# Performance work log

Measured on AMD Instinct MI355X. Metric: run time of the kernel, lower is better.

Reference implementation:

```python
import jax, jax.numpy as jnp
import numpy as np

B, INPUT, HIDDEN, K = 16384, 3072, 1024, 128
D = HIDDEN // K          # latents per sample
NUM_EMB = K              # NearestEmbed(k, k): codebook (emb_dim=K, num_emb=K)


def setup_inputs() -> dict:
    key = jax.random.key(0)
    ks = jax.random.split(key, 6)
    def lin(k, o, i):
        s = 1.0 / np.sqrt(i)
        return jax.random.uniform(k, (o, i), jnp.float32, -s, s)
    return {
        'x':  jax.random.uniform(ks[0], (B, INPUT), jnp.float32),  # image-like in [0,1)
        'W1': lin(ks[1], 400, INPUT),   'b1': jnp.zeros((400,), jnp.float32),
        'W2': lin(ks[2], HIDDEN, 400),  'b2': jnp.zeros((HIDDEN,), jnp.float32),
        'W3': lin(ks[3], 400, HIDDEN),  'b3': jnp.zeros((400,), jnp.float32),
        'W4': lin(ks[4], INPUT, 400),   'b4': jnp.zeros((INPUT,), jnp.float32),
        'W_emb': jax.random.uniform(ks[5], (K, NUM_EMB), jnp.float32),  # torch.rand init
    }


def quantize(x, W):
    # x: (B, K, D) with the embedding dim on axis 1; W: (K, nE)
    # squared distance expansion == argmin of torch.norm over dim 1
    d = (x * x).sum(1)[:, :, None] \
        - 2.0 * jnp.einsum('bkd,kn->bdn', x, W) \
        + (W * W).sum(0)[None, None, :]          # (B, D, nE)
    idx = jnp.argmin(d, axis=-1)                  # (B, D)
    zq = jnp.transpose(W.T[idx], (0, 2, 1))       # gather -> (B, D, K) -> (B, K, D)
    return zq, idx


def reference(x, W1, b1, W2, b2, W3, b3, W4, b4, W_emb):
    # encode
    h1 = jax.nn.relu(x @ W1.T + b1)
    z_e = (h1 @ W2.T + b2).reshape(B, K, D)
    # VQ lookups (weight_sg / input-detach only matter for backward)
    z_q, _ = quantize(z_e, W_emb)
    emb_o, _ = quantize(z_e, W_emb)
    # decode (flatten latents back to hidden, as the math requires)
    h3 = jax.nn.relu(z_q.reshape(B, HIDDEN) @ W3.T + b3)
    recon = jax.nn.sigmoid(h3 @ W4.T + b4)
    return recon, z_e, emb_o
```

## Files before the change

### kernel.cpp

```cpp
#include <hip/hip_runtime.h>
#include <math.h>


typedef short bf16x8 __attribute__((ext_vector_type(8)));
typedef short short8 __attribute__((ext_vector_type(8)));
typedef float f32x4  __attribute__((ext_vector_type(4)));

#define GAP_T   2e-4
#define FIX_CAP 4096

__device__ __forceinline__ unsigned short f32_to_bf16_rn(float v) {
    union { float f; unsigned u; } c; c.f = v;
    unsigned r = c.u + 0x7FFFu + ((c.u >> 16) & 1u);
    return (unsigned short)(r >> 16);
}
__device__ __forceinline__ float bf16_bits_to_f32(unsigned short b) {
    union { unsigned u; float f; } c; c.u = ((unsigned)b) << 16;
    return c.f;
}
__device__ __forceinline__ void glds16(const short* g, short* l) {
    __builtin_amdgcn_global_load_lds(
        (const __attribute__((address_space(1))) unsigned int*)g,
        (__attribute__((address_space(3))) unsigned int*)l, 16, 0, 0);
}
__device__ __forceinline__ size_t zq_plane_off(int id, int ii) {
    const int mb = id >> 7, r = id & 127;
    const int kt = ii >> 5, kc = ii & 31;
    return ((size_t)(mb * 32 + kt) * 4096)
         + r * 32 + (((kc >> 3) ^ (r & 3)) << 3) + (kc & 7);
}

__global__ __launch_bounds__(256) void prep_all(
    const float* __restrict__ x,
    const float* __restrict__ W1, const float* __restrict__ W2,
    const float* __restrict__ W3, const float* __restrict__ W4,
    const float* __restrict__ Wemb,
    short* __restrict__ xh,  short* __restrict__ xl,
    short* __restrict__ w1h, short* __restrict__ w1l,
    short* __restrict__ w2h, short* __restrict__ w2l,
    short* __restrict__ w3h, short* __restrict__ w4h,
    short* __restrict__ wembpl, double* __restrict__ wn,
    int* __restrict__ flag_cnt)
{
    const int tid = threadIdx.x;
    int bid = blockIdx.x;

    if (bid < 12288) {
        const int kt = bid % 96;
        const int mb = bid / 96;
        const size_t tb = (size_t)bid * 4096;
        for (int ci = tid; ci < 512; ci += 256) {
            const int row = ci >> 2;
            const int sl  = ci & 3;
            const int k0  = ((sl ^ (row & 3)) << 3);
            const float* src = &x[(size_t)(mb * 128 + row) * 3072 + kt * 32 + k0];
            const float4 f0 = *reinterpret_cast<const float4*>(src);
            const float4 f1 = *reinterpret_cast<const float4*>(src + 4);
            const float ff[8] = {f0.x, f0.y, f0.z, f0.w, f1.x, f1.y, f1.z, f1.w};
            short8 h, l;
            #pragma unroll
            for (int e = 0; e < 8; ++e) {
                const unsigned short hb = f32_to_bf16_rn(ff[e]);
                h[e] = (short)hb;
                l[e] = (short)f32_to_bf16_rn(ff[e] - bf16_bits_to_f32(hb));
            }
            *reinterpret_cast<short8*>(&xh[tb + ci * 8]) = h;
            *reinterpret_cast<short8*>(&xl[tb + ci * 8]) = l;
        }
        return;
    }
    bid -= 12288;

    if (bid < 928) {
        const float* Wsrc; int N, K, KT, local; short *hi, *lo;
        if (bid < 384)      { Wsrc = W1; N = 400;  K = 3072; KT = 96; local = bid;       hi = w1h; lo = w1l; }
        else if (bid < 488) { Wsrc = W2; N = 1024; K = 400;  KT = 13; local = bid - 384; hi = w2h; lo = w2l; }
        else if (bid < 616) { Wsrc = W3; N = 400;  K = 1024; KT = 32; local = bid - 488; hi = w3h; lo = nullptr; }
        else                { Wsrc = W4; N = 3072; K = 400;  KT = 13; local = bid - 616; hi = w4h; lo = nullptr; }

        const int kt = local % KT;
        const int nb = local / KT;
        const size_t tb = (size_t)local * 4096;
        for (int ci = tid; ci < 512; ci += 256) {
            const int row = ci >> 2;
            const int sl  = ci & 3;
            const int k0  = ((sl ^ (row & 3)) << 3);
            const int n   = nb * 128 + row;
            const int kk  = kt * 32 + k0;
            float f[8];
            #pragma unroll
            for (int e = 0; e < 8; ++e)
                f[e] = (n < N && kk + e < K) ? Wsrc[(size_t)n * K + kk + e] : 0.f;
            short8 h, l;
            #pragma unroll
            for (int e = 0; e < 8; ++e) {
                const unsigned short hb = f32_to_bf16_rn(f[e]);
                h[e] = (short)hb;
                l[e] = (short)f32_to_bf16_rn(f[e] - bf16_bits_to_f32(hb));
            }
            *reinterpret_cast<short8*>(&hi[tb + ci * 8]) = h;
            if (lo) *reinterpret_cast<short8*>(&lo[tb + ci * 8]) = l;
        }
        return;
    }

    if (tid == 0) *flag_cnt = 0;
    if (tid < 128) {
        double s = 0.0;
        for (int k = 0; k < 128; ++k) {
            const double w = (double)Wemb[k * 128 + tid];
            s = fma(w, w, s);
        }
        wn[tid] = s;
    }
    for (int t = tid; t < 16384; t += 256) {
        const int k = t >> 7, n = t & 127;
        const float w = Wemb[t];
        const unsigned short hi = f32_to_bf16_rn(w);
        const unsigned short lo = f32_to_bf16_rn(w - bf16_bits_to_f32(hi));
        const int off = n * 128 + (((k >> 3) ^ (n & 7)) << 3) + (k & 7);
        wembpl[off]         = (short)hi;
        wembpl[16384 + off] = (short)lo;
    }
}

template<int NSPLIT, int ACT, int OUTMODE>
__global__ __launch_bounds__(256) void gemm_pl(
    const short* __restrict__ Ahi, const short* __restrict__ Alo,
    const short* __restrict__ Bhi, const short* __restrict__ Blo,
    const float* __restrict__ bias,
    float* __restrict__ Cf32, short* __restrict__ Cphi, short* __restrict__ Cplo,
    int N, int KT, int KTout)
{
    __shared__ short lds[2 * NSPLIT * 2 * 4096];

    const int tid  = threadIdx.x;
    const int lane = tid & 63;
    const int w_id = tid >> 6;
    const int wr   = (w_id >> 1) * 64;
    const int wc   = (w_id & 1)  * 64;
    const int m0   = blockIdx.y * 128;
    const int n0   = blockIdx.x * 128;
    const int l15  = lane & 15;
    const int lg   = lane >> 4;
    constexpr int BUF = NSPLIT * 2 * 4096;

    f32x4 acc[4][4];
    #pragma unroll
    for (int i = 0; i < 4; ++i)
        #pragma unroll
        for (int j = 0; j < 4; ++j) acc[i][j] = (f32x4){0.f, 0.f, 0.f, 0.f};

    auto stage = [&](int buf, int kt) {
        short* L = &lds[buf * BUF];
        const size_t at = ((size_t)blockIdx.y * KT + kt) * 4096;
        const size_t bt = ((size_t)blockIdx.x * KT + kt) * 4096;
        #pragma unroll
        for (int q = 0; q < 2; ++q) {
            const int o = (w_id * 2 + q) * 512 + lane * 8;
            glds16(Ahi + at + o, &L[o]);
            if (NSPLIT > 1) glds16(Alo + at + o, &L[4096 + o]);
            glds16(Bhi + bt + o, &L[NSPLIT * 4096 + o]);
            if (NSPLIT > 1) glds16(Blo + bt + o, &L[(NSPLIT + 1) * 4096 + o]);
        }
    };

    stage(0, 0);
    __syncthreads();

    int cur = 0;
    for (int kt = 0; kt < KT; ++kt) {
        if (kt + 1 < KT) stage(cur ^ 1, kt + 1);

        const short* L = &lds[cur * BUF];
        bf16x8 bfr[4][NSPLIT];
        #pragma unroll
        for (int fc = 0; fc < 4; ++fc) {
            const int rn  = wc + fc * 16 + l15;
            const int idx = rn * 32 + ((lg ^ (rn & 3)) << 3);
            #pragma unroll
            for (int s = 0; s < NSPLIT; ++s)
                bfr[fc][s] = *reinterpret_cast<const bf16x8*>(&L[(NSPLIT + s) * 4096 + idx]);
        }
        #pragma unroll
        for (int fr = 0; fr < 4; ++fr) {
            const int rm  = wr + fr * 16 + l15;
            const int idx = rm * 32 + ((lg ^ (rm & 3)) << 3);
            const bf16x8 a0 = *reinterpret_cast<const bf16x8*>(&L[idx]);
            bf16x8 a1;
            if (NSPLIT > 1)
                a1 = *reinterpret_cast<const bf16x8*>(&L[4096 + idx]);
            #pragma unroll
            for (int fc = 0; fc < 4; ++fc) {
                acc[fr][fc] = __builtin_amdgcn_mfma_f32_16x16x32_bf16(
                    a0, bfr[fc][0], acc[fr][fc], 0, 0, 0);
                if (NSPLIT > 1) {
                    acc[fr][fc] = __builtin_amdgcn_mfma_f32_16x16x32_bf16(
                        a0, bfr[fc][1], acc[fr][fc], 0, 0, 0);
                    acc[fr][fc] = __builtin_amdgcn_mfma_f32_16x16x32_bf16(
                        a1, bfr[fc][0], acc[fr][fc], 0, 0, 0);
                }
            }
        }
        __syncthreads();
        cur ^= 1;
    }

    float bv[4];
    #pragma unroll
    for (int fc = 0; fc < 4; ++fc) {
        const int col = n0 + wc + fc * 16 + l15;
        bv[fc] = (col < N) ? bias[col] : 0.f;
    }
    #pragma unroll
    for (int fr = 0; fr < 4; ++fr) {
        #pragma unroll
        for (int fc = 0; fc < 4; ++fc) {
            const int col = n0 + wc + fc * 16 + l15;
            #pragma unroll
            for (int j = 0; j < 4; ++j) {
                const int rowg = m0 + wr + fr * 16 + lg * 4 + j;
                float v = acc[fr][fc][j] + bv[fc];
                if (ACT == 1) v = fmaxf(v, 0.f);
                else if (ACT == 2) v = 1.f / (1.f + expf(-v));
                if (OUTMODE == 0) {
                    if (col < N) Cf32[(size_t)rowg * N + col] = v;
                } else {
                    const int kto = col >> 5;
                    if (kto < KTout) {
                        const int r = rowg & 127, k = col & 31;
                        const size_t off = ((size_t)blockIdx.y * KTout + kto) * 4096
                                         + r * 32 + (((k >> 3) ^ (r & 3)) << 3) + (k & 7);
                        const unsigned short hb = f32_to_bf16_rn(v);
                        Cphi[off] = (short)hb;
                        if (OUTMODE == 2)
                            Cplo[off] = (short)f32_to_bf16_rn(v - bf16_bits_to_f32(hb));
                    }
                }
            }
        }
    }
}

__global__ __launch_bounds__(512) void vq_mfma(
    const float* __restrict__ z_e, const short* __restrict__ planes,
    const double* __restrict__ wn_g, float* __restrict__ zq,
    short* __restrict__ zqh,
    int* __restrict__ flag_cnt, int* __restrict__ flag_ids)
{
    __shared__ short  Wsh[32768];
    __shared__ float  zsh[16 * 1024];
    __shared__ double wn_sh[128];
    __shared__ double cmb_v1[128][2];
    __shared__ double cmb_v2[128][2];
    __shared__ int    cmb_i[128][2];
    __shared__ int    idx_sh[128];
    __shared__ int    sflag[16];

    const int tid = threadIdx.x;
    const int b0  = blockIdx.x * 16;

    for (int c = tid; c < 4096; c += 512)
        *reinterpret_cast<int4*>(&Wsh[c * 8]) =
            *reinterpret_cast<const int4*>(&planes[c * 8]);
    for (int c = tid; c < 128; c += 512) wn_sh[c] = wn_g[c];
    for (int c = tid; c < 4096; c += 512) {
        const int D    = c * 16;
        const int s    = D >> 12;
        const int dr   = D & 4095;
        const int srcb = dr ^ (((dr >> 8) & 3) << 5);
        *reinterpret_cast<int4*>(reinterpret_cast<char*>(zsh) + D) =
            *reinterpret_cast<const int4*>(
                reinterpret_cast<const char*>(z_e) + (size_t)(b0 + s) * 4096 + srcb);
    }
    if (tid < 16) sflag[tid] = 0;
    __syncthreads();

    const int lane = tid & 63;
    const int w_id = tid >> 6;
    const int wr   = (w_id >> 1) * 32;
    const int wc   = (w_id & 1) * 64;
    const int l15  = lane & 15;
    const int lg   = lane >> 4;

    f32x4 acc[2][4];
    #pragma unroll
    for (int i = 0; i < 2; ++i)
        #pragma unroll
        for (int j = 0; j < 4; ++j) acc[i][j] = (f32x4){0.f, 0.f, 0.f, 0.f};

    #pragma unroll
    for (int ks = 0; ks < 4; ++ks) {
        bf16x8 bh[4], bl[4];
        #pragma unroll
        for (int cf = 0; cf < 4; ++cf) {
            const int n     = wc + cf * 16 + l15;
            const int slotp = (ks * 4 + lg) ^ (n & 7);
            const int off   = n * 128 + slotp * 8;
            bh[cf] = *reinterpret_cast<const bf16x8*>(&Wsh[off]);
            bl[cf] = *reinterpret_cast<const bf16x8*>(&Wsh[16384 + off]);
        }
        bf16x8 ah[2], al[2];
        #pragma unroll
        for (int rf = 0; rf < 2; ++rf) {
            const int row   = wr + rf * 16 + l15;
            const int s_loc = row >> 3;
            const int d     = row & 7;
            const int kb    = ks * 32 + lg * 8;
            const int xr    = (lg & 3) << 5;
            const char* zb  = reinterpret_cast<const char*>(zsh) + s_loc * 4096;
            bf16x8 h8, L8;
            #pragma unroll
            for (int j = 0; j < 8; ++j) {
                const float a = *reinterpret_cast<const float*>(
                    zb + ((32 * (kb + j) + 4 * d) ^ xr));
                const unsigned short hi = f32_to_bf16_rn(a);
                h8[j] = (short)hi;
                L8[j] = (short)f32_to_bf16_rn(a - bf16_bits_to_f32(hi));
            }
            ah[rf] = h8; al[rf] = L8;
        }
        #pragma unroll
        for (int rf = 0; rf < 2; ++rf)
            #pragma unroll
            for (int cf = 0; cf < 4; ++cf) {
                acc[rf][cf] = __builtin_amdgcn_mfma_f32_16x16x32_bf16(
                    ah[rf], bh[cf], acc[rf][cf], 0, 0, 0);
                acc[rf][cf] = __builtin_amdgcn_mfma_f32_16x16x32_bf16(
                    ah[rf], bl[cf], acc[rf][cf], 0, 0, 0);
                acc[rf][cf] = __builtin_amdgcn_mfma_f32_16x16x32_bf16(
                    al[rf], bh[cf], acc[rf][cf], 0, 0, 0);
            }
    }

    #pragma unroll
    for (int rf = 0; rf < 2; ++rf)
        #pragma unroll
        for (int j = 0; j < 4; ++j) {
            double v1 = 1e300, v2 = 1e300; int i1 = 0;
            #pragma unroll
            for (int cf = 0; cf < 4; ++cf) {
                const int n = wc + cf * 16 + l15;
                const double v = wn_sh[n] - 2.0 * (double)acc[rf][cf][j];
                if (v < v1)      { v2 = v1; v1 = v; i1 = n; }
                else if (v < v2) { v2 = v; }
            }
            #pragma unroll
            for (int off = 1; off < 16; off <<= 1) {
                const double ov1 = __shfl_xor(v1, off);
                const int    oi1 = __shfl_xor(i1, off);
                const double ov2 = __shfl_xor(v2, off);
                if (ov1 < v1 || (ov1 == v1 && oi1 < i1)) {
                    v2 = fmin(v1, ov2); v1 = ov1; i1 = oi1;
                } else {
                    v2 = fmin(v2, ov1);
                }
            }
            if (l15 == 0) {
                const int r = wr + rf * 16 + lg * 4 + j;
                cmb_v1[r][w_id & 1] = v1;
                cmb_v2[r][w_id & 1] = v2;
                cmb_i [r][w_id & 1] = i1;
            }
        }
    __syncthreads();

    if (tid < 128) {
        const double v1a = cmb_v1[tid][0], v1b = cmb_v1[tid][1];
        double v1, v2; int i1;
        if (v1b < v1a) { v1 = v1b; i1 = cmb_i[tid][1]; v2 = fmin(v1a, cmb_v2[tid][1]); }
        else           { v1 = v1a; i1 = cmb_i[tid][0]; v2 = fmin(v1b, cmb_v2[tid][0]); }
        idx_sh[tid] = i1;
        if (v2 - v1 < GAP_T) sflag[tid >> 3] = 1;
    }
    __syncthreads();
    if (tid < 16 && sflag[tid]) {
        const int p = atomicAdd(flag_cnt, 1);
        flag_ids[p] = b0 + tid;
    }

    for (int t = tid; t < 16384; t += 512) {
        const int s = t >> 10, i = t & 1023;
        const int k = i >> 3, d = i & 7;
        const int n = idx_sh[(s << 3) | d];
        const int off = n * 128 + (((k >> 3) ^ (n & 7)) << 3) + (k & 7);
        const float val = bf16_bits_to_f32((unsigned short)Wsh[off]) +
                          bf16_bits_to_f32((unsigned short)Wsh[16384 + off]);
        zq[(size_t)(b0 + s) * 1024 + i] = val;
        zqh[zq_plane_off(b0 + s, i)] = (short)f32_to_bf16_rn(val);
    }
}

#define FLP 68
template<bool GATHER, bool SPLITK, bool FUSERED, typename TA>
__global__ __launch_bounds__(256) void gemm_f64t(
    const TA* __restrict__ A, const float* __restrict__ Wf,
    const int* __restrict__ ids, const int* __restrict__ cntp,
    const float* __restrict__ biasA, const float* __restrict__ bias,
    double* __restrict__ C,
    int AK, int N, int CN, int klen, int cap)
{
    __shared__ double As[16 * FLP];
    __shared__ double Ws[16 * FLP];

    const int tid = threadIdx.x;
    const int tx  = tid & 15;
    const int ty  = tid >> 4;
    const int m0  = blockIdx.y * 64;
    const int n0  = blockIdx.x * 64;
    const int cnt = (*cntp < cap) ? *cntp : cap;
    if (m0 >= cnt) return;

    const int k0 = SPLITK ? blockIdx.z * klen : 0;
    if (SPLITK) C += (size_t)blockIdx.z * cap * CN;

    const int srow = tid >> 2;
    const int sc4  = (tid & 3) << 2;

    const TA* arow;
    if (GATHER) {
        const int m  = m0 + srow;
        const int id = (m < cnt) ? ids[m] : 0;
        arow = A + (size_t)id * AK;
    } else {
        arow = A + (size_t)(m0 + srow) * AK;
    }
    const int   nrow = n0 + srow;
    const float* wrow = Wf + (size_t)(nrow < N ? nrow : 0) * AK;
    const bool  wok  = (nrow < N);

    double acc[4][4];
    #pragma unroll
    for (int i = 0; i < 4; ++i)
        #pragma unroll
        for (int j = 0; j < 4; ++j) acc[i][j] = 0.0;

    for (int kt = 0; kt < klen; kt += 16) {
        const int kb = k0 + kt + sc4;
        if constexpr (FUSERED) {
            const size_t cs = (size_t)cap * AK;
            #pragma unroll
            for (int e = 0; e < 4; ++e) {
                double s = (double)biasA[kb + e];
                #pragma unroll
                for (int c = 0; c < 6; ++c) s += arow[c * cs + kb + e];
                As[(sc4 + e) * FLP + srow] = s > 0.0 ? s : 0.0;
            }
        } else if constexpr (sizeof(TA) == 4) {
            const float4 v = *reinterpret_cast<const float4*>(&arow[kb]);
            As[(sc4 + 0) * FLP + srow] = (double)v.x;
            As[(sc4 + 1) * FLP + srow] = (double)v.y;
            As[(sc4 + 2) * FLP + srow] = (double)v.z;
            As[(sc4 + 3) * FLP + srow] = (double)v.w;
        } else {
            const double2 v0 = *reinterpret_cast<const double2*>(&arow[kb]);
            const double2 v1 = *reinterpret_cast<const double2*>(&arow[kb + 2]);
            As[(sc4 + 0) * FLP + srow] = v0.x;
            As[(sc4 + 1) * FLP + srow] = v0.y;
            As[(sc4 + 2) * FLP + srow] = v1.x;
            As[(sc4 + 3) * FLP + srow] = v1.y;
        }
        float4 w = make_float4(0.f, 0.f, 0.f, 0.f);
        if (wok) w = *reinterpret_cast<const float4*>(&wrow[kb]);
        Ws[(sc4 + 0) * FLP + srow] = (double)w.x;
        Ws[(sc4 + 1) * FLP + srow] = (double)w.y;
        Ws[(sc4 + 2) * FLP + srow] = (double)w.z;
        Ws[(sc4 + 3) * FLP + srow] = (double)w.w;
        __syncthreads();

        #pragma unroll
        for (int k = 0; k < 16; ++k) {
            const double2 A0 = *reinterpret_cast<const double2*>(&As[k * FLP + ty * 4]);
            const double2 A1 = *reinterpret_cast<const double2*>(&As[k * FLP + ty * 4 + 2]);
            const double2 B0 = *reinterpret_cast<const double2*>(&Ws[k * FLP + tx * 4]);
            const double2 B1 = *reinterpret_cast<const double2*>(&Ws[k * FLP + tx * 4 + 2]);
            const double a[4] = {A0.x, A0.y, A1.x, A1.y};
            const double b[4] = {B0.x, B0.y, B1.x, B1.y};
            #pragma unroll
            for (int i = 0; i < 4; ++i)
                #pragma unroll
                for (int j = 0; j < 4; ++j)
                    acc[i][j] = fma(a[i], b[j], acc[i][j]);
        }
        __syncthreads();
    }

    #pragma unroll
    for (int i = 0; i < 4; ++i) {
        const int row = m0 + ty * 4 + i;
        #pragma unroll
        for (int j = 0; j < 4; ++j) {
            const int col = n0 + tx * 4 + j;
            if (col < N)
                C[(size_t)row * CN + col] =
                    acc[i][j] + (bias ? (double)bias[col] : 0.0);
        }
    }
}

__global__ __launch_bounds__(512) void fix_argmin(
    const double* __restrict__ Zf, const float* __restrict__ Wemb,
    const int* __restrict__ cntp, const int* __restrict__ ids,
    float* __restrict__ zq, short* __restrict__ zqh, int cap)
{
    __shared__ float  wesh[16384];
    __shared__ double zsh[4][1032];
    __shared__ double dist[4 * 8 * 128];
    __shared__ int    idxf[32];

    const int tid  = threadIdx.x;
    const int lane = tid & 63;
    const int wv   = tid >> 6;
    const int cnt  = (*cntp < cap) ? *cntp : cap;
    const int base = blockIdx.x * 4;
    if (base >= cnt) return;
    const int ns = (cnt - base < 4) ? (cnt - base) : 4;

    for (int i = tid; i < 4096; i += 512)
        reinterpret_cast<float4*>(wesh)[i] =
            reinterpret_cast<const float4*>(Wemb)[i];
    for (int i = tid; i < 4 * 512; i += 512) {
        const int s = i >> 9, e = (i & 511) * 2;
        if (s < ns) {
            const double2 v = *reinterpret_cast<const double2*>(
                &Zf[(size_t)(base + s) * 1024 + e]);
            zsh[s][e] = v.x;
            zsh[s][e + 1] = v.y;
        }
    }
    __syncthreads();

    for (int t = tid; t < ns * 1024; t += 512) {
        const int s = t >> 10, d = (t >> 7) & 7, n = t & 127;
        double acc = 0.0;
        for (int k = 0; k < 128; ++k) {
            const double diff = zsh[s][k * 8 + d] - (double)wesh[k * 128 + n];
            acc = fma(diff, diff, acc);
        }
        dist[(s * 8 + d) * 128 + n] = acc;
    }
    __syncthreads();

    for (int p = wv; p < ns * 8; p += 8) {
        const double* dp = &dist[p * 128];
        double v0 = dp[lane], vx = dp[lane + 64];
        double v; int ix;
        if (vx < v0) { v = vx; ix = lane + 64; }
        else         { v = v0; ix = lane; }
        #pragma unroll
        for (int off = 32; off > 0; off >>= 1) {
            const double ov = __shfl_down(v, off);
            const int    oi = __shfl_down(ix, off);
            if (ov < v || (ov == v && oi < ix)) { v = ov; ix = oi; }
        }
        if (lane == 0) idxf[p] = ix;
    }
    __syncthreads();

    for (int i = tid; i < ns * 1024; i += 512) {
        const int s = i >> 10, ii = i & 1023;
        const int id = ids[base + s];
        const float val = wesh[(ii >> 3) * 128 + idxf[s * 8 + (ii & 7)]];
        zq[(size_t)id * 1024 + ii] = val;
        zqh[zq_plane_off(id, ii)] = (short)f32_to_bf16_rn(val);
    }
}

extern "C" void kernel_launch(void* const* d_in, const int* in_sizes, int n_in,
                              void* d_out, int out_size, void* d_ws, size_t ws_size,
                              hipStream_t stream)
{
    const float* x    = (const float*)d_in[0];
    const float* W1   = (const float*)d_in[1];
    const float* b1   = (const float*)d_in[2];
    const float* W2   = (const float*)d_in[3];
    const float* b2   = (const float*)d_in[4];
    const float* W3   = (const float*)d_in[5];
    const float* b3   = (const float*)d_in[6];
    const float* W4   = (const float*)d_in[7];
    const float* b4   = (const float*)d_in[8];
    const float* Wemb = (const float*)d_in[9];

    const int B = 16384;
    float* out   = (float*)d_out;
    float* recon = out;
    float* z_e   = out + (size_t)B * 3072;
    float* emb_o = z_e + (size_t)B * 1024;

    constexpr size_t X_PL  = 50331648;
    constexpr size_t H1_PL = 6815744;
    constexpr size_t H3_PL = 6815744;
    constexpr size_t W1_PL = 1572864;
    constexpr size_t W2_PL = 425984;
    constexpr size_t W3_PL = 524288;
    constexpr size_t W4_PL = 1277952;

    short* xh  = (short*)recon;
    short* xl  = xh + X_PL;
    short* h1h = (short*)emb_o;
    short* h1l = h1h + H1_PL;

    short*  h3h      = (short*)d_ws;
    short*  w1h      = h3h + H3_PL;
    short*  w1l      = w1h + W1_PL;
    short*  w2h      = w1l + W1_PL;
    short*  w2l      = w2h + W2_PL;
    short*  w3h      = w2l + W2_PL;
    short*  w4h      = w3h + W3_PL;
    short*  wembpl   = w4h + W4_PL;
    double* wn       = (double*)(wembpl + 32768);
    int*    flag_cnt = (int*)(wn + 128);
    int*    flag_ids = flag_cnt + 64;

    char*   scr  = (char*)recon;
    double* Part = (double*)scr;
    double* Zf   = (double*)(scr + (96ull  << 20));
    short*  zqh  = (short*) (scr + (144ull << 20));

    prep_all<<<dim3(13217), dim3(256), 0, stream>>>(
        x, W1, W2, W3, W4, Wemb, xh, xl, w1h, w1l, w2h, w2l, w3h, w4h,
        wembpl, wn, flag_cnt);

    gemm_pl<2, 1, 2><<<dim3(4, 128), dim3(256), 0, stream>>>(
        xh, xl, w1h, w1l, b1, nullptr, h1h, h1l, 400, 96, 13);
    gemm_pl<2, 0, 0><<<dim3(8, 128), dim3(256), 0, stream>>>(
        h1h, h1l, w2h, w2l, b2, z_e, nullptr, nullptr, 1024, 13, 0);

    vq_mfma<<<dim3(1024), dim3(512), 0, stream>>>(z_e, wembpl, wn, emb_o, zqh,
                                                  flag_cnt, flag_ids);
    gemm_f64t<true, true, false, float><<<dim3(7, FIX_CAP / 64, 6), dim3(256), 0, stream>>>(
        x, W1, flag_ids, flag_cnt, nullptr, nullptr, Part, 3072, 400, 400, 512, FIX_CAP);
    gemm_f64t<false, false, true, double><<<dim3(16, FIX_CAP / 64), dim3(256), 0, stream>>>(
        Part, W2, nullptr, flag_cnt, b1, b2, Zf, 400, 1024, 1024, 400, FIX_CAP);
    fix_argmin<<<dim3(FIX_CAP / 4), dim3(512), 0, stream>>>(
        Zf, Wemb, flag_cnt, flag_ids, emb_o, zqh, FIX_CAP);

    gemm_pl<1, 1, 1><<<dim3(4, 128), dim3(256), 0, stream>>>(
        zqh, nullptr, w3h, nullptr, b3, nullptr, h3h, nullptr, 400, 32, 13);
    gemm_pl<1, 2, 0><<<dim3(24, 128), dim3(256), 0, stream>>>(
        h3h, nullptr, w4h, nullptr, b4, recon, nullptr, nullptr, 3072, 13, 0);
}
```

Measured before the change: 679.4 us.

## Fuse fp32 input split into first GEMM's A-tile loading

Drops the standalone pass that converted x into swizzled bf16 hi/lo planes. GEMM1 now loads fp32 x tiles into registers, splits them into hi/lo bf16 and writes them to LDS while the current tile's MFMAs run. This removes a large read/write pass over the input. In exchange, A loads go through registers instead of direct-to-LDS, and the conversion is repeated for each N-block.

```diff
diff --git a/kernel.cpp b/kernel.cpp
--- a/kernel.cpp
+++ b/kernel.cpp
@@ -31,11 +31,9 @@
 }
 
 __global__ __launch_bounds__(256) void prep_all(
-    const float* __restrict__ x,
     const float* __restrict__ W1, const float* __restrict__ W2,
     const float* __restrict__ W3, const float* __restrict__ W4,
     const float* __restrict__ Wemb,
-    short* __restrict__ xh,  short* __restrict__ xl,
     short* __restrict__ w1h, short* __restrict__ w1l,
     short* __restrict__ w2h, short* __restrict__ w2l,
     short* __restrict__ w3h, short* __restrict__ w4h,
@@ -43,33 +41,7 @@
     int* __restrict__ flag_cnt)
 {
     const int tid = threadIdx.x;
-    int bid = blockIdx.x;
-
-    if (bid < 12288) {
-        const int kt = bid % 96;
-        const int mb = bid / 96;
-        const size_t tb = (size_t)bid * 4096;
-        for (int ci = tid; ci < 512; ci += 256) {
-            const int row = ci >> 2;
-            const int sl  = ci & 3;
-            const int k0  = ((sl ^ (row & 3)) << 3);
-            const float* src = &x[(size_t)(mb * 128 + row) * 3072 + kt * 32 + k0];
-            const float4 f0 = *reinterpret_cast<const float4*>(src);
-            const float4 f1 = *reinterpret_cast<const float4*>(src + 4);
-            const float ff[8] = {f0.x, f0.y, f0.z, f0.w, f1.x, f1.y, f1.z, f1.w};
-            short8 h, l;
-            #pragma unroll
-            for (int e = 0; e < 8; ++e) {
-                const unsigned short hb = f32_to_bf16_rn(ff[e]);
-                h[e] = (short)hb;
-                l[e] = (short)f32_to_bf16_rn(ff[e] - bf16_bits_to_f32(hb));
-            }
-            *reinterpret_cast<short8*>(&xh[tb + ci * 8]) = h;
-            *reinterpret_cast<short8*>(&xl[tb + ci * 8]) = l;
-        }
-        return;
-    }
-    bid -= 12288;
+    const int bid = blockIdx.x;
 
     if (bid < 928) {
         const float* Wsrc; int N, K, KT, local; short *hi, *lo;
@@ -124,9 +96,10 @@
     }
 }
 
-template<int NSPLIT, int ACT, int OUTMODE>
+template<int NSPLIT, int ACT, int AMODE, int OUTMODE>
 __global__ __launch_bounds__(256) void gemm_pl(
     const short* __restrict__ Ahi, const short* __restrict__ Alo,
+    const float* __restrict__ Af32, int AK,
     const short* __restrict__ Bhi, const short* __restrict__ Blo,
     const float* __restrict__ bias,
     float* __restrict__ Cf32, short* __restrict__ Cphi, short* __restrict__ Cplo,
@@ -151,26 +124,68 @@
         #pragma unroll
         for (int j = 0; j < 4; ++j) acc[i][j] = (f32x4){0.f, 0.f, 0.f, 0.f};
 
-    auto stage = [&](int buf, int kt) {
+    float xr[AMODE == 1 ? 16 : 1];
+
+    auto loadA = [&](int kt) {
+        #pragma unroll
+        for (int i = 0; i < 2; ++i) {
+            const int ci  = tid + i * 256;
+            const int row = ci >> 2;
+            const int sl  = ci & 3;
+            const int k0  = ((sl ^ (row & 3)) << 3);
+            const float* src = &Af32[(size_t)(m0 + row) * AK + kt * 32 + k0];
+            const float4 f0 = *reinterpret_cast<const float4*>(src);
+            const float4 f1 = *reinterpret_cast<const float4*>(src + 4);
+            xr[i * 8 + 0] = f0.x; xr[i * 8 + 1] = f0.y;
+            xr[i * 8 + 2] = f0.z; xr[i * 8 + 3] = f0.w;
+            xr[i * 8 + 4] = f1.x; xr[i * 8 + 5] = f1.y;
+            xr[i * 8 + 6] = f1.z; xr[i * 8 + 7] = f1.w;
+        }
+    };
+    auto writeA = [&](int buf) {
         short* L = &lds[buf * BUF];
-        const size_t at = ((size_t)blockIdx.y * KT + kt) * 4096;
+        #pragma unroll
+        for (int i = 0; i < 2; ++i) {
+            const int ci = tid + i * 256;
+            short8 h, l;
+            #pragma unroll
+            for (int e = 0; e < 8; ++e) {
+                const float v = xr[i * 8 + e];
+                const unsigned short hb = f32_to_bf16_rn(v);
+                h[e] = (short)hb;
+                l[e] = (short)f32_to_bf16_rn(v - bf16_bits_to_f32(hb));
+            }
+            *reinterpret_cast<short8*>(&L[ci * 8])        = h;
+            *reinterpret_cast<short8*>(&L[4096 + ci * 8]) = l;
+        }
+    };
+    auto stageGL = [&](int buf, int kt) {
+        short* L = &lds[buf * BUF];
         const size_t bt = ((size_t)blockIdx.x * KT + kt) * 4096;
         #pragma unroll
         for (int q = 0; q < 2; ++q) {
             const int o = (w_id * 2 + q) * 512 + lane * 8;
-            glds16(Ahi + at + o, &L[o]);
-            if (NSPLIT > 1) glds16(Alo + at + o, &L[4096 + o]);
+            if (AMODE == 0) {
+                const size_t at = ((size_t)blockIdx.y * KT + kt) * 4096;
+                glds16(Ahi + at + o, &L[o]);
+                if (NSPLIT > 1) glds16(Alo + at + o, &L[4096 + o]);
+            }
             glds16(Bhi + bt + o, &L[NSPLIT * 4096 + o]);
             if (NSPLIT > 1) glds16(Blo + bt + o, &L[(NSPLIT + 1) * 4096 + o]);
         }
     };
 
-    stage(0, 0);
+    if (AMODE == 1) loadA(0);
+    stageGL(0, 0);
+    if (AMODE == 1) writeA(0);
     __syncthreads();
 
     int cur = 0;
     for (int kt = 0; kt < KT; ++kt) {
-        if (kt + 1 < KT) stage(cur ^ 1, kt + 1);
+        if (kt + 1 < KT) {
+            if (AMODE == 1) loadA(kt + 1);
+            stageGL(cur ^ 1, kt + 1);
+        }
 
         const short* L = &lds[cur * BUF];
         bf16x8 bfr[4][NSPLIT];
@@ -202,6 +217,8 @@
                 }
             }
         }
+
+        if (AMODE == 1 && kt + 1 < KT) writeA(cur ^ 1);
         __syncthreads();
         cur ^= 1;
     }
@@ -587,7 +604,6 @@
     float* z_e   = out + (size_t)B * 3072;
     float* emb_o = z_e + (size_t)B * 1024;
 
-    constexpr size_t X_PL  = 50331648;
     constexpr size_t H1_PL = 6815744;
     constexpr size_t H3_PL = 6815744;
     constexpr size_t W1_PL = 1572864;
@@ -595,8 +611,6 @@
     constexpr size_t W3_PL = 524288;
     constexpr size_t W4_PL = 1277952;
 
-    short* xh  = (short*)recon;
-    short* xl  = xh + X_PL;
     short* h1h = (short*)emb_o;
     short* h1l = h1h + H1_PL;
 
@@ -617,14 +631,14 @@
     double* Zf   = (double*)(scr + (96ull  << 20));
     short*  zqh  = (short*) (scr + (144ull << 20));
 
-    prep_all<<<dim3(13217), dim3(256), 0, stream>>>(
-        x, W1, W2, W3, W4, Wemb, xh, xl, w1h, w1l, w2h, w2l, w3h, w4h,
+    prep_all<<<dim3(929), dim3(256), 0, stream>>>(
+        W1, W2, W3, W4, Wemb, w1h, w1l, w2h, w2l, w3h, w4h,
         wembpl, wn, flag_cnt);
 
-    gemm_pl<2, 1, 2><<<dim3(4, 128), dim3(256), 0, stream>>>(
-        xh, xl, w1h, w1l, b1, nullptr, h1h, h1l, 400, 96, 13);
-    gemm_pl<2, 0, 0><<<dim3(8, 128), dim3(256), 0, stream>>>(
-        h1h, h1l, w2h, w2l, b2, z_e, nullptr, nullptr, 1024, 13, 0);
+    gemm_pl<2, 1, 1, 2><<<dim3(4, 128), dim3(256), 0, stream>>>(
+        nullptr, nullptr, x, 3072, w1h, w1l, b1, nullptr, h1h, h1l, 400, 96, 13);
+    gemm_pl<2, 0, 0, 0><<<dim3(8, 128), dim3(256), 0, stream>>>(
+        h1h, h1l, nullptr, 0, w2h, w2l, b2, z_e, nullptr, nullptr, 1024, 13, 0);
 
     vq_mfma<<<dim3(1024), dim3(512), 0, stream>>>(z_e, wembpl, wn, emb_o, zqh,
                                                   flag_cnt, flag_ids);
@@ -635,8 +649,10 @@
     fix_argmin<<<dim3(FIX_CAP / 4), dim3(512), 0, stream>>>(
         Zf, Wemb, flag_cnt, flag_ids, emb_o, zqh, FIX_CAP);
 
-    gemm_pl<1, 1, 1><<<dim3(4, 128), dim3(256), 0, stream>>>(
-        zqh, nullptr, w3h, nullptr, b3, nullptr, h3h, nullptr, 400, 32, 13);
-    gemm_pl<1, 2, 0><<<dim3(24, 128), dim3(256), 0, stream>>>(
-        h3h, nullptr, w4h, nullptr, b4, recon, nullptr, nullptr, 3072, 13, 0);
-}
+    gemm_pl<1, 1, 0, 1><<<dim3(4, 128), dim3(256), 0, stream>>>(
+        zqh, nullptr, nullptr, 0, w3h, nullptr, b3, nullptr, h3h, nullptr,
+        400, 32, 13);
+    gemm_pl<1, 2, 0, 0><<<dim3(24, 128), dim3(256), 0, stream>>>(
+        h3h, nullptr, nullptr, 0, w4h, nullptr, b4, recon, nullptr, nullptr,
+        3072, 13, 0);
+}
```

After: 670.1 us. No clear change (-1.4%).
